# Kernel optimization log

Hardware: AMD Instinct MI355X
Metric: run time of the kernel (lower is better)

The kernel has to match this reference:

```python
import jax, jax.numpy as jnp
import numpy as np

B, T, MAX_ITEMS = 128, 50, 32
NUM_PRODUCT, E, EW = 100000, 128, 16
D = E + EW  # rnn input/hidden size


def setup_inputs() -> dict:
    key = jax.random.key(0)
    ks = jax.random.split(key, 10)
    # items: 0 is padding; keep roughly half the slots padded (ragged baskets)
    items = jax.random.randint(ks[0], (B, T, MAX_ITEMS), 1, NUM_PRODUCT)
    keep = jax.random.uniform(ks[1], (B, T, MAX_ITEMS)) < 0.5
    keep = keep.at[:, :, 0].set(True)  # at least one item per basket
    items = jnp.where(keep, items, 0)
    flag = jax.random.randint(ks[2], (B, T, 1), 0, 2)
    x = jnp.concatenate([items, flag], axis=-1)  # [B,T,MAX_ITEMS+1], last col = flag
    lengths = jnp.full((B,), T, dtype=jnp.int64)
    hidden = jnp.zeros((1, B, D), dtype=jnp.float32)
    s_e = 1.0 / np.sqrt(E)
    s_d = 1.0 / np.sqrt(D)
    encode_w = jax.random.uniform(ks[3], (NUM_PRODUCT, E), minval=-0.1, maxval=0.1)
    encode_w = encode_w.at[0].set(0.0)  # padding_idx=0
    wchange_w = jax.random.normal(ks[4], (2, EW)) * 0.1
    wchange_w = wchange_w.at[0].set(0.0)  # padding_idx=0
    w_ih = jax.random.uniform(ks[5], (3 * D, D), minval=-s_d, maxval=s_d)
    w_hh = jax.random.uniform(ks[6], (3 * D, D), minval=-s_d, maxval=s_d)
    b_ih = jax.random.uniform(ks[7], (3 * D,), minval=-s_d, maxval=s_d)
    b_hh = jax.random.uniform(ks[8], (3 * D,), minval=-s_d, maxval=s_d)
    fc_w = jax.random.uniform(ks[9], (E, D), minval=-s_d, maxval=s_d)
    fc_b = jnp.zeros((E,), dtype=jnp.float32)
    return {"x": x, "lengths": lengths, "hidden": hidden,
            "encode_w": encode_w, "wchange_w": wchange_w,
            "w_ih": w_ih, "w_hh": w_hh, "b_ih": b_ih, "b_hh": b_hh,
            "fc_w": fc_w, "fc_b": fc_b}


def _embed_baskets(x, encode_w, wchange_w):
    items = x[..., :-1]                      # [B,T,I] product ids, 0 = pad
    flag = x[..., -1]                        # [B,T] 0/1 weight-change flag
    emb = encode_w[items]                    # [B,T,I,E] fused ragged gather
    mask = (items != 0).astype(emb.dtype)[..., None]
    cnt = jnp.maximum(mask.sum(axis=2), 1.0)
    pooled = (emb * mask).sum(axis=2) / cnt  # avg pool over real items [B,T,E]
    w = wchange_w[flag]                      # [B,T,EW]
    return jnp.concatenate([pooled, w], axis=-1)  # [B,T,D]


def _gru(seq, h0, w_ih, w_hh, b_ih, b_hh):
    # seq: [B,T,D], h0: [B,D]; torch GRU cell math
    def step(h, x_t):
        gi = x_t @ w_ih.T + b_ih             # [B,3D]
        gh = h @ w_hh.T + b_hh
        i_r, i_z, i_n = jnp.split(gi, 3, axis=-1)
        h_r, h_z, h_n = jnp.split(gh, 3, axis=-1)
        r = jax.nn.sigmoid(i_r + h_r)
        z = jax.nn.sigmoid(i_z + h_z)
        n = jnp.tanh(i_n + r * h_n)
        h_new = (1.0 - z) * n + z * h
        return h_new, h_new
    h_last, outs = jax.lax.scan(step, h0, jnp.swapaxes(seq, 0, 1))
    return jnp.swapaxes(outs, 0, 1), h_last  # [B,T,D], [B,D]


def reference(x, lengths, hidden, encode_w, wchange_w, w_ih, w_hh, b_ih, b_hh, fc_w, fc_b):
    seq = _embed_baskets(x, encode_w, wchange_w)         # [B,T,D]
    out, h_last = _gru(seq, hidden[0], w_ih, w_hh, b_ih, b_hh)
    dynamic_user = out @ fc_w.T + fc_b                   # [B,T,E]
    return dynamic_user, h_last[None]                    # h_u: [1,B,D]
```

## Files before the change

### kernel.cpp

```cpp
#include <hip/hip_runtime.h>
#include <math.h>

#define B_   128
#define T_   50
#define MI_  32
#define E_   128
#define EW_  16
#define D_   144
#define G_   432
#define N_   (B_*T_)

__global__ __launch_bounds__(256) void embed_kernel(
    const int* __restrict__ x,
    const float* __restrict__ encode_w,
    const float* __restrict__ wchange_w,
    float* __restrict__ seq)
{
    int n = blockIdx.x;
    int tid = threadIdx.x;
    int i = tid >> 3;
    int j = tid & 7;

    __shared__ int xi[33];
    __shared__ __align__(16) float part[32 * 132];
    __shared__ float cntf[32];

    if (tid < 33) xi[tid] = x[n * 33 + tid];
    __syncthreads();

    int it = xi[i];
    const float* row = &encode_w[(size_t)it * E_];
    float4 v0 = *(const float4*)&row[16 * j + 0];
    float4 v1 = *(const float4*)&row[16 * j + 4];
    float4 v2 = *(const float4*)&row[16 * j + 8];
    float4 v3 = *(const float4*)&row[16 * j + 12];

    float* p = &part[i * 132 + 16 * j];
    *(float4*)&p[0]  = v0;
    *(float4*)&p[4]  = v1;
    *(float4*)&p[8]  = v2;
    *(float4*)&p[12] = v3;
    if (j == 0) cntf[i] = (it != 0) ? 1.f : 0.f;
    __syncthreads();

    if (tid < E_) {
        int c = tid;
        float s = 0.f, cn = 0.f;
        #pragma unroll
        for (int k = 0; k < 32; ++k) {
            s  += part[k * 132 + c];
            cn += cntf[k];
        }
        seq[n * D_ + c] = s / fmaxf(cn, 1.f);
    } else if (tid < E_ + EW_) {
        int c = tid - E_;
        seq[n * D_ + E_ + c] = wchange_w[xi[32] * EW_ + c];
    }
}

#define GK   144
#define GBK  48
#define GPAD 68

__global__ __launch_bounds__(256) void gemm_bias_kernel(
    const float* __restrict__ A,
    const float* __restrict__ Bw,
    const float* __restrict__ bias,
    float* __restrict__ C,
    int M, int N)
{
    __shared__ float As[GBK * GPAD];
    __shared__ float Bs[GBK * GPAD];

    int tid = threadIdx.x;
    int row0 = blockIdx.x * 64;
    int col0 = blockIdx.y * 64;
    int tx = tid & 15;
    int ty = tid >> 4;

    float acc[4][4] = {};

    int sr = tid >> 2;
    int skq0 = tid & 3;

    for (int k0 = 0; k0 < GK; k0 += GBK) {
        __syncthreads();
        #pragma unroll
        for (int i = 0; i < 3; ++i) {
            int kq = skq0 + i * 4;
            float4 a = *(const float4*)&A[(size_t)(row0 + sr) * GK + k0 + kq * 4];
            int nrow = col0 + sr;
            float4 b = make_float4(0.f, 0.f, 0.f, 0.f);
            if (nrow < N)
                b = *(const float4*)&Bw[(size_t)nrow * GK + k0 + kq * 4];
            As[(kq * 4 + 0) * GPAD + sr] = a.x;
            As[(kq * 4 + 1) * GPAD + sr] = a.y;
            As[(kq * 4 + 2) * GPAD + sr] = a.z;
            As[(kq * 4 + 3) * GPAD + sr] = a.w;
            Bs[(kq * 4 + 0) * GPAD + sr] = b.x;
            Bs[(kq * 4 + 1) * GPAD + sr] = b.y;
            Bs[(kq * 4 + 2) * GPAD + sr] = b.z;
            Bs[(kq * 4 + 3) * GPAD + sr] = b.w;
        }
        __syncthreads();

        #pragma unroll 4
        for (int k = 0; k < GBK; ++k) {
            float4 a4 = *(const float4*)&As[k * GPAD + ty * 4];
            float4 b4 = *(const float4*)&Bs[k * GPAD + tx * 4];
            float av[4] = {a4.x, a4.y, a4.z, a4.w};
            float bv[4] = {b4.x, b4.y, b4.z, b4.w};
            #pragma unroll
            for (int i = 0; i < 4; ++i)
                #pragma unroll
                for (int j = 0; j < 4; ++j)
                    acc[i][j] = fmaf(av[i], bv[j], acc[i][j]);
        }
    }

    int c = col0 + tx * 4;
    if (c < N) {
        float4 bb = *(const float4*)&bias[c];
        #pragma unroll
        for (int i = 0; i < 4; ++i) {
            int r = row0 + ty * 4 + i;
            float4 o;
            o.x = acc[i][0] + bb.x;
            o.y = acc[i][1] + bb.y;
            o.z = acc[i][2] + bb.z;
            o.w = acc[i][3] + bb.w;
            *(float4*)&C[(size_t)r * N + c] = o;
        }
    }
}

template<int CTRL>
__device__ __forceinline__ float dpp_xor_add(float x) {
    int y = __builtin_amdgcn_mov_dpp(__float_as_int(x), CTRL, 0xF, 0xF, true);
    return x + __int_as_float(y);
}

__global__ __launch_bounds__(576) void gru_kernel(
    const float* __restrict__ gi,
    const float* __restrict__ w_hh,
    const float* __restrict__ b_hh,
    const float* __restrict__ h0,
    float* __restrict__ hseq,
    float* __restrict__ hlast)
{
    int b = blockIdx.x;
    int tid = threadIdx.x;
    int g = tid >> 3;
    int s = tid & 7;
    int k0 = s * 20;

    __shared__ __align__(16) float h[160];
    __shared__ float gh[G_];

    float w[6][20];
    #pragma unroll
    for (int r = 0; r < 6; ++r) {
        const float* wrow = &w_hh[(size_t)(6 * g + r) * D_];
        #pragma unroll
        for (int q = 0; q < 5; ++q) {
            int k = k0 + 4 * q;
            float4 t = make_float4(0.f, 0.f, 0.f, 0.f);
            if (k < D_) t = *(const float4*)&wrow[k];
            w[r][4 * q + 0] = t.x;
            w[r][4 * q + 1] = t.y;
            w[r][4 * q + 2] = t.z;
            w[r][4 * q + 3] = t.w;
        }
    }
    float bias = (s < 6) ? b_hh[6 * g + s] : 0.f;

    if (tid < 160) h[tid] = (tid < D_) ? h0[b * D_ + tid] : 0.f;
    __syncthreads();

    for (int t = 0; t < T_; ++t) {
        int n = b * T_ + t;
        float gir = 0.f, giz = 0.f, gin = 0.f;
        if (tid < D_) {
            gir = gi[(size_t)n * G_ + tid];
            giz = gi[(size_t)n * G_ + D_ + tid];
            gin = gi[(size_t)n * G_ + 2 * D_ + tid];
        }

        float hv[20];
        #pragma unroll
        for (int q = 0; q < 5; ++q) {
            float4 t4 = *(const float4*)&h[k0 + 4 * q];
            hv[4 * q + 0] = t4.x;
            hv[4 * q + 1] = t4.y;
            hv[4 * q + 2] = t4.z;
            hv[4 * q + 3] = t4.w;
        }

        float a0 = 0.f, a1 = 0.f, a2 = 0.f, a3 = 0.f, a4 = 0.f, a5 = 0.f;
        #pragma unroll
        for (int kk = 0; kk < 20; ++kk) {
            float hk = hv[kk];
            a0 = fmaf(w[0][kk], hk, a0);
            a1 = fmaf(w[1][kk], hk, a1);
            a2 = fmaf(w[2][kk], hk, a2);
            a3 = fmaf(w[3][kk], hk, a3);
            a4 = fmaf(w[4][kk], hk, a4);
            a5 = fmaf(w[5][kk], hk, a5);
        }

        a0 = dpp_xor_add<0xB1>(a0); a0 = dpp_xor_add<0x4E>(a0); a0 = dpp_xor_add<0x141>(a0);
        a1 = dpp_xor_add<0xB1>(a1); a1 = dpp_xor_add<0x4E>(a1); a1 = dpp_xor_add<0x141>(a1);
        a2 = dpp_xor_add<0xB1>(a2); a2 = dpp_xor_add<0x4E>(a2); a2 = dpp_xor_add<0x141>(a2);
        a3 = dpp_xor_add<0xB1>(a3); a3 = dpp_xor_add<0x4E>(a3); a3 = dpp_xor_add<0x141>(a3);
        a4 = dpp_xor_add<0xB1>(a4); a4 = dpp_xor_add<0x4E>(a4); a4 = dpp_xor_add<0x141>(a4);
        a5 = dpp_xor_add<0xB1>(a5); a5 = dpp_xor_add<0x4E>(a5); a5 = dpp_xor_add<0x141>(a5);

        float myacc = a0;
        if (s == 1) myacc = a1;
        if (s == 2) myacc = a2;
        if (s == 3) myacc = a3;
        if (s == 4) myacc = a4;
        if (s == 5) myacc = a5;
        if (s < 6) gh[6 * g + s] = myacc + bias;
        __syncthreads();

        if (tid < D_) {
            float r = 1.f / (1.f + __expf(-(gir + gh[tid])));
            float z = 1.f / (1.f + __expf(-(giz + gh[D_ + tid])));
            float narg = gin + r * gh[2 * D_ + tid];
            narg = fminf(fmaxf(narg, -15.f), 15.f);
            float e2 = __expf(-2.f * narg);
            float nn = (1.f - e2) / (1.f + e2);
            float hn = (1.f - z) * nn + z * h[tid];
            hseq[(size_t)n * D_ + tid] = hn;
            h[tid] = hn;
        }
        __syncthreads();
    }

    if (tid < D_) hlast[b * D_ + tid] = h[tid];
}

extern "C" void kernel_launch(void* const* d_in, const int* in_sizes, int n_in,
                              void* d_out, int out_size, void* d_ws, size_t ws_size,
                              hipStream_t stream)
{
    const int*   x         = (const int*)d_in[0];
    const float* hidden    = (const float*)d_in[2];
    const float* encode_w  = (const float*)d_in[3];
    const float* wchange_w = (const float*)d_in[4];
    const float* w_ih      = (const float*)d_in[5];
    const float* w_hh      = (const float*)d_in[6];
    const float* b_ih      = (const float*)d_in[7];
    const float* b_hh      = (const float*)d_in[8];
    const float* fc_w      = (const float*)d_in[9];
    const float* fc_b      = (const float*)d_in[10];

    float* out = (float*)d_out;
    float* ws  = (float*)d_ws;
    float* seq  = ws;
    float* gi   = ws + 921600;
    float* hseq = ws + 921600 + 2764800;

    embed_kernel<<<N_, 256, 0, stream>>>(x, encode_w, wchange_w, seq);

    gemm_bias_kernel<<<dim3(N_ / 64, (G_ + 63) / 64), 256, 0, stream>>>(
        seq, w_ih, b_ih, gi, N_, G_);

    gru_kernel<<<B_, 576, 0, stream>>>(gi, w_hh, b_hh, hidden, hseq,
                                       out + (size_t)N_ * E_);

    gemm_bias_kernel<<<dim3(N_ / 64, E_ / 64), 256, 0, stream>>>(
        hseq, fc_w, fc_b, out, N_, E_);
}
```

Baseline: 188.1 us.

## Remap GRU gate rows so each lane group owns its outputs, drop one barrier

Each 8-lane group now holds the r, z and n weight rows for two hidden units rather than six consecutive gate rows, so the reduced gate sums stay in registers and the gate nonlinearity is applied by lanes 0 and 1 of each group directly. This removes the shared gh buffer and one __syncthreads per timestep; a double-buffered hidden state keeps the remaining single barrier correct. The gi values for the next step are prefetched into registers during the current step to hide global load latency. In exchange, elementwise work is spread across 144 lanes in strided groups, which costs some intra-wave divergence.

```diff
diff --git a/kernel.cpp b/kernel.cpp
--- a/kernel.cpp
+++ b/kernel.cpp
@@ -153,14 +153,15 @@
     int g = tid >> 3;
     int s = tid & 7;
     int k0 = s * 20;
-
-    __shared__ __align__(16) float h[160];
-    __shared__ float gh[G_];
+    int e = 2 * g + (s & 1);
+
+    __shared__ __align__(16) float hb[2][160];
 
     float w[6][20];
     #pragma unroll
     for (int r = 0; r < 6; ++r) {
-        const float* wrow = &w_hh[(size_t)(6 * g + r) * D_];
+        int rowi = (r >> 1) * D_ + 2 * g + (r & 1);
+        const float* wrow = &w_hh[(size_t)rowi * D_];
         #pragma unroll
         for (int q = 0; q < 5; ++q) {
             int k = k0 + 4 * q;
@@ -172,24 +173,48 @@
             w[r][4 * q + 3] = t.w;
         }
     }
-    float bias = (s < 6) ? b_hh[6 * g + s] : 0.f;
-
-    if (tid < 160) h[tid] = (tid < D_) ? h0[b * D_ + tid] : 0.f;
+    float br = 0.f, bz = 0.f, bn = 0.f;
+    if (s < 2) {
+        br = b_hh[e];
+        bz = b_hh[D_ + e];
+        bn = b_hh[2 * D_ + e];
+    }
+
+    if (tid < 160) {
+        hb[0][tid] = (tid < D_) ? h0[b * D_ + tid] : 0.f;
+        hb[1][tid] = 0.f;
+    }
     __syncthreads();
 
+    float gir = 0.f, giz = 0.f, ginv = 0.f;
+    if (s < 2) {
+        const float* gp = &gi[(size_t)(b * T_) * G_];
+        gir  = gp[e];
+        giz  = gp[D_ + e];
+        ginv = gp[2 * D_ + e];
+    }
+
+    int cur = 0;
+    float hn_last = 0.f;
     for (int t = 0; t < T_; ++t) {
         int n = b * T_ + t;
-        float gir = 0.f, giz = 0.f, gin = 0.f;
-        if (tid < D_) {
-            gir = gi[(size_t)n * G_ + tid];
-            giz = gi[(size_t)n * G_ + D_ + tid];
-            gin = gi[(size_t)n * G_ + 2 * D_ + tid];
+
+        float girU = gir, gizU = giz, ginU = ginv;
+        float hold = 0.f;
+        if (s < 2) {
+            hold = hb[cur][e];
+            if (t + 1 < T_) {
+                const float* gp = &gi[(size_t)(n + 1) * G_];
+                gir  = gp[e];
+                giz  = gp[D_ + e];
+                ginv = gp[2 * D_ + e];
+            }
         }
 
         float hv[20];
         #pragma unroll
         for (int q = 0; q < 5; ++q) {
-            float4 t4 = *(const float4*)&h[k0 + 4 * q];
+            float4 t4 = *(const float4*)&hb[cur][k0 + 4 * q];
             hv[4 * q + 0] = t4.x;
             hv[4 * q + 1] = t4.y;
             hv[4 * q + 2] = t4.z;
@@ -215,30 +240,29 @@
         a4 = dpp_xor_add<0xB1>(a4); a4 = dpp_xor_add<0x4E>(a4); a4 = dpp_xor_add<0x141>(a4);
         a5 = dpp_xor_add<0xB1>(a5); a5 = dpp_xor_add<0x4E>(a5); a5 = dpp_xor_add<0x141>(a5);
 
-        float myacc = a0;
-        if (s == 1) myacc = a1;
-        if (s == 2) myacc = a2;
-        if (s == 3) myacc = a3;
-        if (s == 4) myacc = a4;
-        if (s == 5) myacc = a5;
-        if (s < 6) gh[6 * g + s] = myacc + bias;
-        __syncthreads();
-
-        if (tid < D_) {
-            float r = 1.f / (1.f + __expf(-(gir + gh[tid])));
-            float z = 1.f / (1.f + __expf(-(giz + gh[D_ + tid])));
-            float narg = gin + r * gh[2 * D_ + tid];
+        if (s < 2) {
+            float ar = (s == 0) ? a0 : a1;
+            float az = (s == 0) ? a2 : a3;
+            float an = (s == 0) ? a4 : a5;
+            float ghr = ar + br;
+            float ghz = az + bz;
+            float ghn = an + bn;
+            float rr = 1.f / (1.f + __expf(-(girU + ghr)));
+            float zz = 1.f / (1.f + __expf(-(gizU + ghz)));
+            float narg = ginU + rr * ghn;
             narg = fminf(fmaxf(narg, -15.f), 15.f);
             float e2 = __expf(-2.f * narg);
             float nn = (1.f - e2) / (1.f + e2);
-            float hn = (1.f - z) * nn + z * h[tid];
-            hseq[(size_t)n * D_ + tid] = hn;
-            h[tid] = hn;
+            float hn = (1.f - zz) * nn + zz * hold;
+            hseq[(size_t)n * D_ + e] = hn;
+            hb[cur ^ 1][e] = hn;
+            hn_last = hn;
         }
         __syncthreads();
-    }
-
-    if (tid < D_) hlast[b * D_ + tid] = h[tid];
+        cur ^= 1;
+    }
+
+    if (s < 2) hlast[b * D_ + e] = hn_last;
 }
 
 extern "C" void kernel_launch(void* const* d_in, const int* in_sizes, int n_in,
```

After: 188.0 us. About the same (-0.1%).

## Fuse output FC projection into GRU recurrence kernel

Applied to the files above, without the earlier changes.

Computes the fc projection of each hidden state inside the GRU kernel, reusing the h vector already loaded for the recurrent matvec. Warps 0-63 hold fc_w rows in registers and emit step t-1's output during step t, with a final epilogue for the last step. This removes the hseq round-trip through memory and the separate fc GEMM launch. In exchange it adds register pressure (40 more floats per thread at 576 threads) and extra FMAs on the serial critical path of every step.

```diff
diff --git a/kernel.cpp b/kernel.cpp
--- a/kernel.cpp
+++ b/kernel.cpp
@@ -145,7 +145,9 @@
     const float* __restrict__ w_hh,
     const float* __restrict__ b_hh,
     const float* __restrict__ h0,
-    float* __restrict__ hseq,
+    const float* __restrict__ fc_w,
+    const float* __restrict__ fc_b,
+    float* __restrict__ dyn,
     float* __restrict__ hlast)
 {
     int b = blockIdx.x;
@@ -174,6 +176,23 @@
     }
     float bias = (s < 6) ? b_hh[6 * g + s] : 0.f;
 
+    float wf[2][20];
+    #pragma unroll
+    for (int r = 0; r < 2; ++r) {
+        #pragma unroll
+        for (int q = 0; q < 5; ++q) {
+            int k = k0 + 4 * q;
+            float4 t = make_float4(0.f, 0.f, 0.f, 0.f);
+            if (g < 64 && k < D_)
+                t = *(const float4*)&fc_w[(size_t)(2 * g + r) * D_ + k];
+            wf[r][4 * q + 0] = t.x;
+            wf[r][4 * q + 1] = t.y;
+            wf[r][4 * q + 2] = t.z;
+            wf[r][4 * q + 3] = t.w;
+        }
+    }
+    float fbias = (g < 64 && s < 2) ? fc_b[2 * g + s] : 0.f;
+
     if (tid < 160) h[tid] = (tid < D_) ? h0[b * D_ + tid] : 0.f;
     __syncthreads();
 
@@ -222,6 +241,20 @@
         if (s == 4) myacc = a4;
         if (s == 5) myacc = a5;
         if (s < 6) gh[6 * g + s] = myacc + bias;
+
+        if (g < 64) {
+            float f0 = 0.f, f1 = 0.f;
+            #pragma unroll
+            for (int kk = 0; kk < 20; ++kk) {
+                float hk = hv[kk];
+                f0 = fmaf(wf[0][kk], hk, f0);
+                f1 = fmaf(wf[1][kk], hk, f1);
+            }
+            f0 = dpp_xor_add<0xB1>(f0); f0 = dpp_xor_add<0x4E>(f0); f0 = dpp_xor_add<0x141>(f0);
+            f1 = dpp_xor_add<0xB1>(f1); f1 = dpp_xor_add<0x4E>(f1); f1 = dpp_xor_add<0x141>(f1);
+            if (t > 0 && s < 2)
+                dyn[(size_t)(n - 1) * E_ + 2 * g + s] = ((s == 0) ? f0 : f1) + fbias;
+        }
         __syncthreads();
 
         if (tid < D_) {
@@ -232,12 +265,33 @@
             float e2 = __expf(-2.f * narg);
             float nn = (1.f - e2) / (1.f + e2);
             float hn = (1.f - z) * nn + z * h[tid];
-            hseq[(size_t)n * D_ + tid] = hn;
             h[tid] = hn;
         }
         __syncthreads();
     }
 
+    if (g < 64) {
+        float hv[20];
+        #pragma unroll
+        for (int q = 0; q < 5; ++q) {
+            float4 t4 = *(const float4*)&h[k0 + 4 * q];
+            hv[4 * q + 0] = t4.x;
+            hv[4 * q + 1] = t4.y;
+            hv[4 * q + 2] = t4.z;
+            hv[4 * q + 3] = t4.w;
+        }
+        float f0 = 0.f, f1 = 0.f;
+        #pragma unroll
+        for (int kk = 0; kk < 20; ++kk) {
+            float hk = hv[kk];
+            f0 = fmaf(wf[0][kk], hk, f0);
+            f1 = fmaf(wf[1][kk], hk, f1);
+        }
+        f0 = dpp_xor_add<0xB1>(f0); f0 = dpp_xor_add<0x4E>(f0); f0 = dpp_xor_add<0x141>(f0);
+        f1 = dpp_xor_add<0xB1>(f1); f1 = dpp_xor_add<0x4E>(f1); f1 = dpp_xor_add<0x141>(f1);
+        if (s < 2)
+            dyn[(size_t)(b * T_ + T_ - 1) * E_ + 2 * g + s] = ((s == 0) ? f0 : f1) + fbias;
+    }
     if (tid < D_) hlast[b * D_ + tid] = h[tid];
 }
 
@@ -260,16 +314,12 @@
     float* ws  = (float*)d_ws;
     float* seq  = ws;
     float* gi   = ws + 921600;
-    float* hseq = ws + 921600 + 2764800;
 
     embed_kernel<<<N_, 256, 0, stream>>>(x, encode_w, wchange_w, seq);
 
     gemm_bias_kernel<<<dim3(N_ / 64, (G_ + 63) / 64), 256, 0, stream>>>(
         seq, w_ih, b_ih, gi, N_, G_);
 
-    gru_kernel<<<B_, 576, 0, stream>>>(gi, w_hh, b_hh, hidden, hseq,
-                                       out + (size_t)N_ * E_);
-
-    gemm_bias_kernel<<<dim3(N_ / 64, E_ / 64), 256, 0, stream>>>(
-        hseq, fc_w, fc_b, out, N_, E_);
-}
+    gru_kernel<<<B_, 576, 0, stream>>>(gi, w_hh, b_hh, hidden, fc_w, fc_b,
+                                       out, out + (size_t)N_ * E_);
+}
```

Result: slower. 289.2 us (+53.7%).
